# Kernel optimization log

Hardware: AMD Instinct MI355X
Metric: run time of the kernel (lower is better)

Reference implementation:

```python
import jax, jax.numpy as jnp
import numpy as np

L, C = 256, 20
BATCH = 1024


def _pairwise_mask(L, C, mask_type='pairwise'):
    # mask[l1, c1, l2, c2] nonzero iff positions interact (l2 - l1 >= 1, or == 1 for neighbor)
    ls = jnp.arange(L)
    d = ls[None, :] - ls[:, None]  # [L, L] = l2 - l1
    m = (d >= 1) if mask_type == 'pairwise' else (d == 1)
    return jnp.broadcast_to(m[:, None, :, None], (L, C, L, C)).astype(jnp.float32)


def setup_inputs() -> dict:
    key = jax.random.key(0)
    k1, k2, k3 = jax.random.split(key, 3)
    x_lc = jax.random.uniform(k1, (BATCH, L * C), dtype=jnp.float32)
    theta_0 = jnp.zeros((1,), dtype=jnp.float32)
    theta_lc = jax.random.normal(k2, (L, C), dtype=jnp.float32) / np.sqrt(L)
    theta_lclc = jax.random.normal(k3, (L, C, L, C), dtype=jnp.float32) / np.sqrt(L * L)
    return {"x_lc": x_lc, "theta_0": theta_0, "theta_lc": theta_lc, "theta_lclc": theta_lclc}


def reference(x_lc, theta_0, theta_lc, theta_lclc):
    Ld, Cd = theta_lc.shape
    mask = _pairwise_mask(Ld, Cd, 'pairwise')
    # additive term: sum_lc theta_lc * x_lc  -> [B, 1]
    lin = x_lc @ theta_lc.reshape(Ld * Cd)  # [B]
    # pairwise term: x^T (theta * mask) x, expressed as a masked GEMM instead of a
    # broadcasted [B, L, C, L, C] product
    Theta = (theta_lclc * mask).reshape(Ld * Cd, Ld * Cd)  # [LC, LC]
    xm = x_lc @ Theta  # [B, LC]
    quad = jnp.sum(xm * x_lc, axis=1)  # [B]
    phi = theta_0 + (lin + quad)[:, None]  # [B, 1]
    return phi
```

## Files before the change

kernel.cpp:

```cpp
#include <hip/hip_runtime.h>
#include <hip/hip_bf16.h>
#include <cstdint>
#include <cstddef>

#define LCN 5120
#define BN  1024
#define CN  20

typedef __attribute__((ext_vector_type(4))) float  floatx4;
typedef __attribute__((ext_vector_type(8))) short  shortx8;
typedef __attribute__((ext_vector_type(4))) unsigned short ushortx4;
typedef __attribute__((ext_vector_type(8))) unsigned short ushortx8;

static __device__ __forceinline__ unsigned short f2bf(float f) {
    __hip_bfloat16 h = __float2bfloat16(f);
    return *reinterpret_cast<unsigned short*>(&h);
}

static __device__ __forceinline__ void gload_lds16(const void* g, void* l) {
    __builtin_amdgcn_global_load_lds(
        (const __attribute__((address_space(1))) void*)g,
        (__attribute__((address_space(3))) void*)l,
        16, 0, 0);
}

__global__ __launch_bounds__(256) void k_prep(
    const float* __restrict__ th,
    const float* __restrict__ x,
    const float* __restrict__ th0,
    const float* __restrict__ thlc,
    unsigned short* __restrict__ Tb,
    unsigned short* __restrict__ Xb,
    float*          __restrict__ out)
{
    const int tid = threadIdx.x;
    if (blockIdx.x < LCN / 4) {
        const int w = tid >> 6, lane = tid & 63;
        const int i = blockIdx.x * 4 + w;
        const int lmin = ((i >> 8) << 8) / CN;
        const int js   = 1024 * ((CN * (lmin + 1)) / 1024);
        const int jmin = CN * (i / CN) + CN;
        const float* src = th + (size_t)i * LCN;
        unsigned short* dst = Tb + (size_t)i * LCN;
        for (int j = js + lane * 8; j < LCN; j += 512) {
            const floatx4 v0 = *reinterpret_cast<const floatx4*>(src + j);
            const floatx4 v1 = *reinterpret_cast<const floatx4*>(src + j + 4);
            ushortx8 o;
#pragma unroll
            for (int e = 0; e < 4; ++e) o[e]     = (j + e     >= jmin) ? f2bf(v0[e]) : (unsigned short)0;
#pragma unroll
            for (int e = 0; e < 4; ++e) o[4 + e] = (j + 4 + e >= jmin) ? f2bf(v1[e]) : (unsigned short)0;
            *reinterpret_cast<ushortx8*>(dst + j) = o;
        }
    } else {
        const int b = blockIdx.x - LCN / 4;
        const floatx4* xr = reinterpret_cast<const floatx4*>(x + (size_t)b * LCN);
        const floatx4* tr = reinterpret_cast<const floatx4*>(thlc);
        ushortx4* xw = reinterpret_cast<ushortx4*>(Xb + (size_t)b * LCN);
        float s = 0.0f;
        for (int k = tid; k < LCN / 4; k += 256) {
            const floatx4 a = xr[k], t2 = tr[k];
            s += a[0] * t2[0] + a[1] * t2[1] + a[2] * t2[2] + a[3] * t2[3];
            ushortx4 o;
#pragma unroll
            for (int e = 0; e < 4; ++e) o[e] = f2bf(a[e]);
            xw[k] = o;
        }
#pragma unroll
        for (int off = 32; off > 0; off >>= 1) s += __shfl_down(s, off, 64);
        __shared__ float ws4[4];
        if ((tid & 63) == 0) ws4[tid >> 6] = s;
        __syncthreads();
        if (tid == 0) out[b] = th0[0] + ws4[0] + ws4[1] + ws4[2] + ws4[3];
    }
}

__global__ __launch_bounds__(512, 2) void k_quad(
    const unsigned short* __restrict__ Xb,
    const unsigned short* __restrict__ Tb,
    float*                __restrict__ out)
{
    const int bid  = blockIdx.x;
    const int xcd  = bid & 7;
    const int slot = bid >> 3;
    const int m    = slot & 3;
    const int cl   = slot >> 2;
    int qc = cl * 8 + xcd;
    if (qc >= 60) return;

    int n = 0, cs = 0;
    for (int t = 0; t < 20; ++t) {
        const int lmin = (256 * t) / CN;
        const int c0   = (CN * (lmin + 1)) / 1024;
        const int cnt  = 5 - c0;
        if (qc < cnt) { n = t; cs = c0 + qc; break; }
        qc -= cnt;
    }
    const int b0 = m * 256;
    const int n0 = n * 256;
    const int k0 = cs * 1024;

    __shared__ unsigned short As[4 * 256 * 32];
    __shared__ unsigned short Bs[4 * 256 * 32];
    __shared__ float partial[256];

    const int tid  = threadIdx.x;
    const int lane = tid & 63;
    const int w    = tid >> 6;
    const int wm   = w & 1;
    const int wn   = w >> 1;
    const int lrow = lane & 15;
    const int kq   = lane >> 4;

    if (tid < 256) partial[tid] = 0.0f;

    floatx4 acc[8][4];
#pragma unroll
    for (int mt = 0; mt < 8; ++mt)
#pragma unroll
        for (int nt = 0; nt < 4; ++nt) acc[mt][nt] = (floatx4)0.0f;

    int aoff[8], boff[4];
#pragma unroll
    for (int mt = 0; mt < 8; ++mt) {
        const int row = wm * 128 + mt * 16 + lrow;
        aoff[mt] = row * 32 + (((kq + (row >> 1)) & 3) << 3);
    }
#pragma unroll
    for (int nt = 0; nt < 4; ++nt) {
        const int row = wn * 64 + nt * 16 + lrow;
        boff[nt] = row * 32 + (((kq + (row >> 1)) & 3) << 3);
    }

#define STAGE(buf, kc) do {                                                       \
    _Pragma("unroll")                                                             \
    for (int t = 0; t < 2; ++t) {                                                 \
        const int s    = t * 512 + tid;                                           \
        const int row  = s >> 2;                                                  \
        const int gseg = ((s & 3) - (row >> 1)) & 3;                              \
        char* la = (char*)As + (buf) * 16384 + (size_t)(t * 512 + w * 64) * 16;   \
        char* lb = (char*)Bs + (buf) * 16384 + (size_t)(t * 512 + w * 64) * 16;   \
        gload_lds16(Xb + (size_t)(b0 + row) * LCN + (kc) + gseg * 8, la);         \
        gload_lds16(Tb + (size_t)(n0 + row) * LCN + (kc) + gseg * 8, lb);         \
    }                                                                             \
} while (0)

#define BODY(kk, PAR, VM) do {                                                     \
    asm volatile("s_waitcnt vmcnt(" #VM ")" ::: "memory");                         \
    __builtin_amdgcn_s_barrier();                                                  \
    if ((kk) + 3 < 32) STAGE(((PAR) + 3) & 3, k0 + ((kk) + 3) * 32);               \
    shortx8 bf4[4], af8[8];                                                        \
    _Pragma("unroll")                                                              \
    for (int nt = 0; nt < 4; ++nt)                                                 \
        bf4[nt] = *reinterpret_cast<const shortx8*>(Bs + (PAR) * 8192 + boff[nt]); \
    _Pragma("unroll")                                                              \
    for (int mt = 0; mt < 8; ++mt)                                                 \
        af8[mt] = *reinterpret_cast<const shortx8*>(As + (PAR) * 8192 + aoff[mt]); \
    __builtin_amdgcn_s_setprio(1);                                                 \
    _Pragma("unroll")                                                              \
    for (int mt = 0; mt < 8; ++mt)                                                 \
        _Pragma("unroll")                                                          \
        for (int nt = 0; nt < 4; ++nt)                                             \
            acc[mt][nt] = __builtin_amdgcn_mfma_f32_16x16x32_bf16(af8[mt], bf4[nt], acc[mt][nt], 0, 0, 0); \
    __builtin_amdgcn_s_setprio(0);                                                 \
} while (0)

    STAGE(0, k0);
    STAGE(1, k0 + 32);
    STAGE(2, k0 + 64);

    for (int kk = 0; kk < 28; kk += 4) {
        BODY(kk + 0, 0, 8);
        BODY(kk + 1, 1, 8);
        BODY(kk + 2, 2, 8);
        BODY(kk + 3, 3, 8);
    }
    BODY(28, 0, 8);
    BODY(29, 1, 8);
    BODY(30, 2, 4);
    BODY(31, 3, 0);
#undef BODY
#undef STAGE

#pragma unroll
    for (int mt = 0; mt < 8; ++mt) {
#pragma unroll
        for (int r = 0; r < 4; ++r) {
            const int b = b0 + wm * 128 + mt * 16 + kq * 4 + r;
            float s = 0.0f;
#pragma unroll
            for (int nt = 0; nt < 4; ++nt) {
                const int i = n0 + wn * 64 + nt * 16 + lrow;
                const __hip_bfloat16 hv = *reinterpret_cast<const __hip_bfloat16*>(&Xb[(size_t)b * LCN + i]);
                s += acc[mt][nt][r] * __bfloat162float(hv);
            }
            s += __shfl_xor(s, 1, 64);
            s += __shfl_xor(s, 2, 64);
            s += __shfl_xor(s, 4, 64);
            s += __shfl_xor(s, 8, 64);
            if (lrow == 0) atomicAdd(&partial[b - b0], s);
        }
    }
    __syncthreads();
    if (tid < 256) atomicAdd(&out[b0 + tid], partial[tid]);
}

extern "C" void kernel_launch(void* const* d_in, const int* in_sizes, int n_in,
                              void* d_out, int out_size, void* d_ws, size_t ws_size,
                              hipStream_t stream) {
    const float* x      = (const float*)d_in[0];
    const float* th0    = (const float*)d_in[1];
    const float* thlc   = (const float*)d_in[2];
    const float* thlclc = (const float*)d_in[3];
    float* out = (float*)d_out;

    unsigned short* Tb = (unsigned short*)d_ws;
    unsigned short* Xb = (unsigned short*)((char*)d_ws + (size_t)LCN * LCN * 2);

    k_prep<<<dim3(LCN / 4 + BN), 256, 0, stream>>>(thlclc, x, th0, thlc, Tb, Xb, out);

    k_quad<<<dim3(256), 512, 0, stream>>>(Xb, Tb, out);
}
```

Before: 212.9 us.

## Split each k-tile into two MFMA phases interleaved with staged A/B loads

Restructures the main GEMM loop so each k-tile is processed in two halves: load B fragments and the first half of A fragments, issue the A prefetch, compute, then load the second A half, issue the B prefetch and compute. It adds extra barriers to interleave global-to-LDS loads with MFMA work. It also precomputes per-thread global source pointers that are advanced incrementally, and changes the LDS swizzle from (row>>1) to row. The aim is better overlap of memory traffic with matrix math and lower VGPR pressure from holding fewer A fragments at once, at the cost of extra barrier synchronisation.

```diff
diff --git a/kernel.cpp b/kernel.cpp
--- a/kernel.cpp
+++ b/kernel.cpp
@@ -124,63 +124,93 @@
 #pragma unroll
     for (int mt = 0; mt < 8; ++mt) {
         const int row = wm * 128 + mt * 16 + lrow;
-        aoff[mt] = row * 32 + (((kq + (row >> 1)) & 3) << 3);
+        aoff[mt] = row * 32 + (((kq + row) & 3) << 3);
     }
 #pragma unroll
     for (int nt = 0; nt < 4; ++nt) {
         const int row = wn * 64 + nt * 16 + lrow;
-        boff[nt] = row * 32 + (((kq + (row >> 1)) & 3) << 3);
-    }
-
-#define STAGE(buf, kc) do {                                                       \
+        boff[nt] = row * 32 + (((kq + row) & 3) << 3);
+    }
+
+    const int srow = tid >> 2;
+    const int gseg = ((tid & 3) - (srow & 3)) & 3;
+    const unsigned short* aS[2];
+    const unsigned short* bS[2];
+#pragma unroll
+    for (int r = 0; r < 2; ++r) {
+        aS[r] = Xb + (size_t)(b0 + r * 128 + srow) * LCN + k0 + gseg * 8;
+        bS[r] = Tb + (size_t)(n0 + r * 128 + srow) * LCN + k0 + gseg * 8;
+    }
+
+#define STAGE_A(PAR) do {                                                         \
     _Pragma("unroll")                                                             \
-    for (int t = 0; t < 2; ++t) {                                                 \
-        const int s    = t * 512 + tid;                                           \
-        const int row  = s >> 2;                                                  \
-        const int gseg = ((s & 3) - (row >> 1)) & 3;                              \
-        char* la = (char*)As + (buf) * 16384 + (size_t)(t * 512 + w * 64) * 16;   \
-        char* lb = (char*)Bs + (buf) * 16384 + (size_t)(t * 512 + w * 64) * 16;   \
-        gload_lds16(Xb + (size_t)(b0 + row) * LCN + (kc) + gseg * 8, la);         \
-        gload_lds16(Tb + (size_t)(n0 + row) * LCN + (kc) + gseg * 8, lb);         \
+    for (int r = 0; r < 2; ++r) {                                                 \
+        char* la = (char*)As + (PAR) * 16384 + (size_t)(r * 512 + w * 64) * 16;   \
+        gload_lds16(aS[r], la); aS[r] += 32;                                      \
     }                                                                             \
 } while (0)
 
-#define BODY(kk, PAR, VM) do {                                                     \
+#define STAGE_B(PAR) do {                                                         \
+    _Pragma("unroll")                                                             \
+    for (int r = 0; r < 2; ++r) {                                                 \
+        char* lb = (char*)Bs + (PAR) * 16384 + (size_t)(r * 512 + w * 64) * 16;   \
+        gload_lds16(bS[r], lb); bS[r] += 32;                                      \
+    }                                                                             \
+} while (0)
+
+#define TILE(t_, PAR, VM) do {                                                     \
     asm volatile("s_waitcnt vmcnt(" #VM ")" ::: "memory");                         \
     __builtin_amdgcn_s_barrier();                                                  \
-    if ((kk) + 3 < 32) STAGE(((PAR) + 3) & 3, k0 + ((kk) + 3) * 32);               \
-    shortx8 bf4[4], af8[8];                                                        \
+    const unsigned short* Ab = As + (PAR) * 8192;                                  \
+    const unsigned short* Bb = Bs + (PAR) * 8192;                                  \
+    shortx8 bfv[4], af[4];                                                         \
     _Pragma("unroll")                                                              \
     for (int nt = 0; nt < 4; ++nt)                                                 \
-        bf4[nt] = *reinterpret_cast<const shortx8*>(Bs + (PAR) * 8192 + boff[nt]); \
-    _Pragma("unroll")                                                              \
-    for (int mt = 0; mt < 8; ++mt)                                                 \
-        af8[mt] = *reinterpret_cast<const shortx8*>(As + (PAR) * 8192 + aoff[mt]); \
+        bfv[nt] = *reinterpret_cast<const shortx8*>(Bb + boff[nt]);                \
+    _Pragma("unroll")                                                              \
+    for (int a = 0; a < 4; ++a)                                                    \
+        af[a] = *reinterpret_cast<const shortx8*>(Ab + aoff[a]);                   \
+    if ((t_) + 3 < 32) STAGE_A(((PAR) + 3) & 3);                                   \
+    __builtin_amdgcn_s_barrier();                                                  \
     __builtin_amdgcn_s_setprio(1);                                                 \
     _Pragma("unroll")                                                              \
-    for (int mt = 0; mt < 8; ++mt)                                                 \
+    for (int a = 0; a < 4; ++a)                                                    \
         _Pragma("unroll")                                                          \
         for (int nt = 0; nt < 4; ++nt)                                             \
-            acc[mt][nt] = __builtin_amdgcn_mfma_f32_16x16x32_bf16(af8[mt], bf4[nt], acc[mt][nt], 0, 0, 0); \
+            acc[a][nt] = __builtin_amdgcn_mfma_f32_16x16x32_bf16(af[a], bfv[nt], acc[a][nt], 0, 0, 0); \
+    __builtin_amdgcn_s_setprio(0);                                                 \
+    __builtin_amdgcn_s_barrier();                                                  \
+    _Pragma("unroll")                                                              \
+    for (int a = 0; a < 4; ++a)                                                    \
+        af[a] = *reinterpret_cast<const shortx8*>(Ab + aoff[4 + a]);               \
+    if ((t_) + 3 < 32) STAGE_B(((PAR) + 3) & 3);                                   \
+    __builtin_amdgcn_s_barrier();                                                  \
+    __builtin_amdgcn_s_setprio(1);                                                 \
+    _Pragma("unroll")                                                              \
+    for (int a = 0; a < 4; ++a)                                                    \
+        _Pragma("unroll")                                                          \
+        for (int nt = 0; nt < 4; ++nt)                                             \
+            acc[4 + a][nt] = __builtin_amdgcn_mfma_f32_16x16x32_bf16(af[a], bfv[nt], acc[4 + a][nt], 0, 0, 0); \
     __builtin_amdgcn_s_setprio(0);                                                 \
 } while (0)
 
-    STAGE(0, k0);
-    STAGE(1, k0 + 32);
-    STAGE(2, k0 + 64);
-
-    for (int kk = 0; kk < 28; kk += 4) {
-        BODY(kk + 0, 0, 8);
-        BODY(kk + 1, 1, 8);
-        BODY(kk + 2, 2, 8);
-        BODY(kk + 3, 3, 8);
-    }
-    BODY(28, 0, 8);
-    BODY(29, 1, 8);
-    BODY(30, 2, 4);
-    BODY(31, 3, 0);
-#undef BODY
-#undef STAGE
+    STAGE_A(0); STAGE_B(0);
+    STAGE_A(1); STAGE_B(1);
+    STAGE_A(2); STAGE_B(2);
+
+    for (int t = 0; t < 28; t += 4) {
+        TILE(t + 0, 0, 8);
+        TILE(t + 1, 1, 8);
+        TILE(t + 2, 2, 8);
+        TILE(t + 3, 3, 8);
+    }
+    TILE(28, 0, 8);
+    TILE(29, 1, 8);
+    TILE(30, 2, 4);
+    TILE(31, 3, 0);
+#undef TILE
+#undef STAGE_A
+#undef STAGE_B
 
 #pragma unroll
     for (int mt = 0; mt < 8; ++mt) {
```

Measured after the change: 214.7 us. Within noise of the previous version (+0.9%).

## Fuse prep and quad kernels into one cooperative launch with grid sync

Applied to the files above, without the earlier changes.

Merges the bf16 conversion and linear-term kernel into the GEMM kernel using a cooperative launch and grid-wide sync. Each active block converts exactly the theta tile rows and K-range it will later consume, and every block converts four x rows and computes their linear term. This removes a second kernel launch and the large prep grid, and it converts only the needed theta region. The cost is a grid barrier and conversion work spread over just 256 blocks, with fewer threads doing the prep than before.

```diff
diff --git a/kernel.cpp b/kernel.cpp
--- a/kernel.cpp
+++ b/kernel.cpp
@@ -1,7 +1,10 @@
 #include <hip/hip_runtime.h>
 #include <hip/hip_bf16.h>
+#include <hip/hip_cooperative_groups.h>
 #include <cstdint>
 #include <cstddef>
+
+namespace cg = cooperative_groups;
 
 #define LCN 5120
 #define BN  1024
@@ -9,7 +12,6 @@
 
 typedef __attribute__((ext_vector_type(4))) float  floatx4;
 typedef __attribute__((ext_vector_type(8))) short  shortx8;
-typedef __attribute__((ext_vector_type(4))) unsigned short ushortx4;
 typedef __attribute__((ext_vector_type(8))) unsigned short ushortx8;
 
 static __device__ __forceinline__ unsigned short f2bf(float f) {
@@ -24,77 +26,34 @@
         16, 0, 0);
 }
 
-__global__ __launch_bounds__(256) void k_prep(
-    const float* __restrict__ th,
+__global__ __launch_bounds__(512, 2) void k_fused(
     const float* __restrict__ x,
     const float* __restrict__ th0,
     const float* __restrict__ thlc,
+    const float* __restrict__ th,
     unsigned short* __restrict__ Tb,
     unsigned short* __restrict__ Xb,
     float*          __restrict__ out)
-{
-    const int tid = threadIdx.x;
-    if (blockIdx.x < LCN / 4) {
-        const int w = tid >> 6, lane = tid & 63;
-        const int i = blockIdx.x * 4 + w;
-        const int lmin = ((i >> 8) << 8) / CN;
-        const int js   = 1024 * ((CN * (lmin + 1)) / 1024);
-        const int jmin = CN * (i / CN) + CN;
-        const float* src = th + (size_t)i * LCN;
-        unsigned short* dst = Tb + (size_t)i * LCN;
-        for (int j = js + lane * 8; j < LCN; j += 512) {
-            const floatx4 v0 = *reinterpret_cast<const floatx4*>(src + j);
-            const floatx4 v1 = *reinterpret_cast<const floatx4*>(src + j + 4);
-            ushortx8 o;
-#pragma unroll
-            for (int e = 0; e < 4; ++e) o[e]     = (j + e     >= jmin) ? f2bf(v0[e]) : (unsigned short)0;
-#pragma unroll
-            for (int e = 0; e < 4; ++e) o[4 + e] = (j + 4 + e >= jmin) ? f2bf(v1[e]) : (unsigned short)0;
-            *reinterpret_cast<ushortx8*>(dst + j) = o;
-        }
-    } else {
-        const int b = blockIdx.x - LCN / 4;
-        const floatx4* xr = reinterpret_cast<const floatx4*>(x + (size_t)b * LCN);
-        const floatx4* tr = reinterpret_cast<const floatx4*>(thlc);
-        ushortx4* xw = reinterpret_cast<ushortx4*>(Xb + (size_t)b * LCN);
-        float s = 0.0f;
-        for (int k = tid; k < LCN / 4; k += 256) {
-            const floatx4 a = xr[k], t2 = tr[k];
-            s += a[0] * t2[0] + a[1] * t2[1] + a[2] * t2[2] + a[3] * t2[3];
-            ushortx4 o;
-#pragma unroll
-            for (int e = 0; e < 4; ++e) o[e] = f2bf(a[e]);
-            xw[k] = o;
-        }
-#pragma unroll
-        for (int off = 32; off > 0; off >>= 1) s += __shfl_down(s, off, 64);
-        __shared__ float ws4[4];
-        if ((tid & 63) == 0) ws4[tid >> 6] = s;
-        __syncthreads();
-        if (tid == 0) out[b] = th0[0] + ws4[0] + ws4[1] + ws4[2] + ws4[3];
-    }
-}
-
-__global__ __launch_bounds__(512, 2) void k_quad(
-    const unsigned short* __restrict__ Xb,
-    const unsigned short* __restrict__ Tb,
-    float*                __restrict__ out)
 {
     const int bid  = blockIdx.x;
     const int xcd  = bid & 7;
     const int slot = bid >> 3;
     const int m    = slot & 3;
     const int cl   = slot >> 2;
-    int qc = cl * 8 + xcd;
-    if (qc >= 60) return;
+    const int qc   = cl * 8 + xcd;
+    const bool active = (qc < 60);
+    const int tid  = threadIdx.x;
 
     int n = 0, cs = 0;
-    for (int t = 0; t < 20; ++t) {
-        const int lmin = (256 * t) / CN;
-        const int c0   = (CN * (lmin + 1)) / 1024;
-        const int cnt  = 5 - c0;
-        if (qc < cnt) { n = t; cs = c0 + qc; break; }
-        qc -= cnt;
+    if (active) {
+        int q = qc;
+        for (int t = 0; t < 20; ++t) {
+            const int lmin = (256 * t) / CN;
+            const int c0   = (CN * (lmin + 1)) / 1024;
+            const int cnt  = 5 - c0;
+            if (q < cnt) { n = t; cs = c0 + q; break; }
+            q -= cnt;
+        }
     }
     const int b0 = m * 256;
     const int n0 = n * 256;
@@ -103,8 +62,60 @@
     __shared__ unsigned short As[4 * 256 * 32];
     __shared__ unsigned short Bs[4 * 256 * 32];
     __shared__ float partial[256];
-
-    const int tid  = threadIdx.x;
+    __shared__ float ws8[8];
+
+    if (active) {
+        const int rbase = n0 + m * 64;
+        const int colb  = (tid & 127) * 8;
+        const int rowo  = tid >> 7;
+#pragma unroll 4
+        for (int p = 0; p < 16; ++p) {
+            const int r    = rbase + p * 4 + rowo;
+            const int jmin = (r / CN) * CN + CN;
+            const int j0   = k0 + colb;
+            const float* src = th + (size_t)r * LCN + j0;
+            const floatx4 v0 = *reinterpret_cast<const floatx4*>(src);
+            const floatx4 v1 = *reinterpret_cast<const floatx4*>(src + 4);
+            ushortx8 o;
+#pragma unroll
+            for (int e = 0; e < 4; ++e) {
+                o[e]     = (j0 + e     >= jmin) ? f2bf(v0[e]) : (unsigned short)0;
+                o[4 + e] = (j0 + 4 + e >= jmin) ? f2bf(v1[e]) : (unsigned short)0;
+            }
+            *reinterpret_cast<ushortx8*>(Tb + (size_t)r * LCN + j0) = o;
+        }
+    }
+
+    {
+        const int xr = (bid << 2) + (tid >> 7);
+        const int t2 = tid & 127;
+        const float* xs = x + (size_t)xr * LCN;
+        float s = 0.0f;
+#pragma unroll
+        for (int it = 0; it < 5; ++it) {
+            const int k = it * 1024 + t2 * 8;
+            const floatx4 a0 = *reinterpret_cast<const floatx4*>(xs + k);
+            const floatx4 a1 = *reinterpret_cast<const floatx4*>(xs + k + 4);
+            const floatx4 t0 = *reinterpret_cast<const floatx4*>(thlc + k);
+            const floatx4 t1 = *reinterpret_cast<const floatx4*>(thlc + k + 4);
+            s += a0[0]*t0[0] + a0[1]*t0[1] + a0[2]*t0[2] + a0[3]*t0[3]
+               + a1[0]*t1[0] + a1[1]*t1[1] + a1[2]*t1[2] + a1[3]*t1[3];
+            ushortx8 o;
+#pragma unroll
+            for (int e = 0; e < 4; ++e) { o[e] = f2bf(a0[e]); o[4 + e] = f2bf(a1[e]); }
+            *reinterpret_cast<ushortx8*>(Xb + (size_t)xr * LCN + k) = o;
+        }
+#pragma unroll
+        for (int off = 32; off > 0; off >>= 1) s += __shfl_down(s, off, 64);
+        if ((tid & 63) == 0) ws8[tid >> 6] = s;
+        __syncthreads();
+        if (t2 == 0) out[xr] = th0[0] + ws8[(tid >> 7) * 2] + ws8[(tid >> 7) * 2 + 1];
+    }
+
+    __threadfence();
+    cg::this_grid().sync();
+    if (!active) return;
+
     const int lane = tid & 63;
     const int w    = tid >> 6;
     const int wm   = w & 1;
@@ -217,7 +228,8 @@
     unsigned short* Tb = (unsigned short*)d_ws;
     unsigned short* Xb = (unsigned short*)((char*)d_ws + (size_t)LCN * LCN * 2);
 
-    k_prep<<<dim3(LCN / 4 + BN), 256, 0, stream>>>(thlclc, x, th0, thlc, Tb, Xb, out);
-
-    k_quad<<<dim3(256), 512, 0, stream>>>(Xb, Tb, out);
-}
+    void* args[] = { (void*)&x, (void*)&th0, (void*)&thlc, (void*)&thlclc,
+                     (void*)&Tb, (void*)&Xb, (void*)&out };
+    hipLaunchCooperativeKernel((const void*)k_fused, dim3(256), dim3(512),
+                               args, 0, stream);
+}
```

Measured after the change: 312.8 us. 1.47x slower.
